# Optimization experiments

Hardware: AMD Instinct MI355X
Metric: run time of the kernel (lower is better)

The kernel has to match this reference:

```python
import jax, jax.numpy as jnp
import numpy as np

N_NODES = 100000
N_EDGES = 1600000
N_PAIRS = 500000
IN_C, HID_C, OUT_C = 128, 128, 128


def setup_inputs() -> dict:
    key = jax.random.key(0)
    ks = jax.random.split(key, 12)
    def lin(k, fan_in, shape):
        b = 1.0 / np.sqrt(fan_in)
        return jax.random.uniform(k, shape, jnp.float32, -b, b)
    return {
        "x": jax.random.normal(ks[0], (N_NODES, IN_C), jnp.float32),
        "edge_index": jax.random.randint(ks[1], (2, N_EDGES), 0, N_NODES),
        "edge_pairs": jax.random.randint(ks[2], (2, N_PAIRS), 0, N_NODES),
        "W1": lin(ks[3], IN_C, (IN_C, HID_C)),
        "b1": jnp.zeros((HID_C,), jnp.float32),
        "W2": lin(ks[4], HID_C, (HID_C, OUT_C)),
        "b2": jnp.zeros((OUT_C,), jnp.float32),
        "Wm1": lin(ks[5], 2 * OUT_C, (2 * OUT_C, HID_C)),
        "bm1": lin(ks[6], 2 * OUT_C, (HID_C,)),
        "Wm2": lin(ks[7], HID_C, (HID_C, 1)),
        "bm2": lin(ks[8], HID_C, (1,)),
    }


def reference(x, edge_index, edge_pairs, W1, b1, W2, b2, Wm1, bm1, Wm2, bm2):
    N = x.shape[0]
    loop = jnp.arange(N, dtype=edge_index.dtype)
    row = jnp.concatenate([edge_index[0], loop])  # source nodes (+self loops)
    col = jnp.concatenate([edge_index[1], loop])  # target nodes (+self loops)
    # symmetric GCN normalization: deg^{-1/2}[row] * deg^{-1/2}[col]
    deg = jax.ops.segment_sum(jnp.ones(col.shape, x.dtype), col, num_segments=N)
    dinv = jnp.where(deg > 0, jax.lax.rsqrt(deg), 0.0)
    norm = dinv[row] * dinv[col]  # [E+N]

    def gcn_conv(h, W, b):
        h = h @ W  # transform first (PyG GCNConv lin has no bias)
        msg = h[row] * norm[:, None]
        return jax.ops.segment_sum(msg, col, num_segments=N) + b

    h = jax.nn.relu(gcn_conv(x, W1, b1))
    h = gcn_conv(h, W2, b2)  # dropout p=0.0 -> identity

    src, dst = edge_pairs[0], edge_pairs[1]
    ef = jnp.concatenate([h[src], h[dst]], axis=-1)  # [P, 2*out]
    out = jax.nn.relu(ef @ Wm1 + bm1) @ Wm2 + bm2
    return out.squeeze(-1)
```

## Files before the change

### kernel.cpp

```cpp
#include <hip/hip_runtime.h>
#include <hip/hip_fp16.h>

#define NCH 128
#define G_NODES 256
#define EPB 4096
#define RCAP 4864
#define MAXNB 512
#define KST 40

typedef __attribute__((ext_vector_type(8))) short short8;
typedef _Float16 half8 __attribute__((ext_vector_type(8)));
typedef __attribute__((ext_vector_type(4))) float floatx4;

static inline size_t align256(size_t x){ return (x + 255) & ~(size_t)255; }

__global__ __launch_bounds__(256) void binA_kernel(
    const int* __restrict__ row, const int* __restrict__ col,
    int* __restrict__ gcur, unsigned* __restrict__ bucketed, int E, int NB,
    const float* __restrict__ W1, const float* __restrict__ W2,
    const float* __restrict__ Wm1, short* __restrict__ planes){
  __shared__ int cnt[MAXNB];
  __shared__ int lbase[MAXNB];
  __shared__ int gbase[MAXNB];
  __shared__ unsigned sorted[EPB];
  __shared__ unsigned short binOf[EPB];
  __shared__ int sh[256];
  __shared__ int carry;
  int t = threadIdx.x;
  int e0 = blockIdx.x * EPB;
  int ecnt = min(EPB, E - e0);
  for (int i = t; i < NB; i += 256) cnt[i] = 0;
  if (t == 0) carry = 0;
  __syncthreads();
  unsigned rec[16]; int bn[16]; int rk[16];
  #pragma unroll
  for (int i = 0; i < 16; i++){
    int e = e0 + i * 256 + t;
    if (e < E){
      int r = row[e], c = col[e];
      bn[i]  = c >> 8;
      rec[i] = (unsigned)r | ((unsigned)(c & 255) << 17);
      rk[i]  = atomicAdd(&cnt[bn[i]], 1);
    } else bn[i] = -1;
  }
  __syncthreads();
  for (int start = 0; start < NB; start += 256){
    int i = start + t;
    int v = (i < NB) ? cnt[i] : 0;
    sh[t] = v; __syncthreads();
    for (int off = 1; off < 256; off <<= 1){
      int val = (t >= off) ? sh[t - off] : 0;
      __syncthreads(); sh[t] += val; __syncthreads();
    }
    if (i < NB) lbase[i] = sh[t] - v + carry;
    __syncthreads();
    if (t == 255) carry += sh[255];
    __syncthreads();
  }
  for (int i = t; i < NB; i += 256){
    int c = cnt[i];
    gbase[i] = (c > 0) ? atomicAdd(&gcur[i], c) : 0;
  }
  __syncthreads();
  #pragma unroll
  for (int i = 0; i < 16; i++){
    if (bn[i] >= 0){
      int pos = lbase[bn[i]] + rk[i];
      sorted[pos] = rec[i];
      binOf[pos]  = (unsigned short)bn[i];
    }
  }
  __syncthreads();
  for (int idx = t; idx < ecnt; idx += 256){
    int b = binOf[idx];
    int gpos = gbase[b] + (idx - lbase[b]);
    if (gpos < RCAP) bucketed[(size_t)b * RCAP + gpos] = sorted[idx];
  }
  {
    int gid = blockIdx.x * 256 + t;
    if (gid < 4 * 16384){
      int mat = gid >> 14;
      int idx = gid & 16383;
      int k = idx >> 7, n = idx & 127;
      const float* src = (mat == 0) ? W1 : (mat == 1) ? W2 : (mat == 2) ? Wm1 : (Wm1 + 16384);
      float x = src[idx];
      short hs, ls;
      if (mat == 0){
        unsigned u = __float_as_uint(x);
        hs = (short)(u >> 16);
        float hf = __uint_as_float(u & 0xFFFF0000u);
        ls = (short)(__float_as_uint(x - hf) >> 16);
      } else {
        __half h = __float2half(x);
        __half l = __float2half(x - __half2float(h));
        hs = __half_as_short(h); ls = __half_as_short(l);
      }
      planes[(size_t)(2 * mat) * 16384 + n * 128 + k]     = hs;
      planes[(size_t)(2 * mat + 1) * 16384 + n * 128 + k] = ls;
    }
  }
}

__global__ __launch_bounds__(512, 4) void fused_gemm_binB(
    const float* __restrict__ X, const short* __restrict__ Whi_,
    const short* __restrict__ Wlo_, __half* __restrict__ O, int nrows, int gemmBlocks,
    const unsigned* __restrict__ bucketed, const int* __restrict__ gcur,
    int* __restrict__ rows_sorted, int* __restrict__ offs,
    int* __restrict__ counts, float* __restrict__ dinv, int N){
  __shared__ __align__(16) char smem[40960];
  int t = threadIdx.x;
  if (blockIdx.x < gemmBlocks){
    short* Xhi = (short*)smem;
    short* Xlo = Xhi + 128 * KST;
    short* Whi = Xlo + 128 * KST;
    short* Wlo = Whi + 128 * KST;
    int w = t >> 6, lane = t & 63;
    int m = lane & 15, q = lane >> 4;
    int row0 = blockIdx.x * 128;
    floatx4 acc[8];
    #pragma unroll
    for (int ct = 0; ct < 8; ct++) acc[ct] = (floatx4)0.f;
    for (int kc = 0; kc < 4; kc++){
      int k0 = kc * 32;
      __syncthreads();
      #pragma unroll
      for (int qq = 0; qq < 2; qq++){
        int f = t + 512 * qq;
        int r = f >> 3, kq = f & 7;
        int gr = row0 + r;
        int grc = (gr < nrows) ? gr : 0;
        float4 v = *(const float4*)(X + (size_t)grc * NCH + k0 + kq * 4);
        short h[4], l[4];
        float vv[4] = {v.x, v.y, v.z, v.w};
        #pragma unroll
        for (int j = 0; j < 4; j++){
          unsigned u = __float_as_uint(vv[j]);
          h[j] = (short)(u >> 16);
          float hf = __uint_as_float(u & 0xFFFF0000u);
          l[j] = (short)(__float_as_uint(vv[j] - hf) >> 16);
        }
        *(uint2*)(Xhi + r * KST + kq * 4) = *(uint2*)h;
        *(uint2*)(Xlo + r * KST + kq * 4) = *(uint2*)l;
      }
      {
        int n = t >> 2, kq = t & 3;
        *(uint4*)(Whi + n * KST + kq * 8) = *(const uint4*)(Whi_ + n * NCH + k0 + kq * 8);
        *(uint4*)(Wlo + n * KST + kq * 8) = *(const uint4*)(Wlo_ + n * NCH + k0 + kq * 8);
      }
      __syncthreads();
      short8 a_hi = *(const short8*)(Xhi + (w * 16 + m) * KST + q * 8);
      short8 a_lo = *(const short8*)(Xlo + (w * 16 + m) * KST + q * 8);
      #pragma unroll
      for (int ct = 0; ct < 8; ct++){
        short8 b_hi = *(const short8*)(Whi + (ct * 16 + m) * KST + q * 8);
        short8 b_lo = *(const short8*)(Wlo + (ct * 16 + m) * KST + q * 8);
        acc[ct] = __builtin_amdgcn_mfma_f32_16x16x32_bf16(a_hi, b_hi, acc[ct], 0, 0, 0);
        acc[ct] = __builtin_amdgcn_mfma_f32_16x16x32_bf16(a_lo, b_hi, acc[ct], 0, 0, 0);
        acc[ct] = __builtin_amdgcn_mfma_f32_16x16x32_bf16(a_hi, b_lo, acc[ct], 0, 0, 0);
      }
    }
    #pragma unroll
    for (int r = 0; r < 4; r++){
      int grow = row0 + w * 16 + q * 4 + r;
      if (grow < nrows){
        #pragma unroll
        for (int ct = 0; ct < 8; ct++)
          O[(size_t)grow * NCH + ct * 16 + m] = __float2half(acc[ct][r]);
      }
    }
  } else {
    int b = blockIdx.x - gemmBlocks;
    unsigned* ledge = (unsigned*)smem;
    int* cnt  = (int*)(smem + RCAP * 4);
    int* cnt2 = cnt + 256;
    int* lex  = cnt2 + 256;
    int* sh   = lex + 256;
    int size = min(gcur[b], RCAP);
    int n0 = b * G_NODES;
    if (t < 256){ cnt[t] = 0; cnt2[t] = 0; }
    __syncthreads();
    for (int i = t; i < size; i += 512){
      unsigned v = bucketed[(size_t)b * RCAP + i];
      ledge[i] = v;
      atomicAdd(&cnt[v >> 17], 1);
    }
    __syncthreads();
    {
      int v = (t < 256) ? cnt[t] : 0;
      if (t < 256) sh[t] = v;
      __syncthreads();
      for (int off = 1; off < 256; off <<= 1){
        int val = (t >= off && t < 256) ? sh[t - off] : 0;
        __syncthreads();
        if (t < 256) sh[t] += val;
        __syncthreads();
      }
      if (t < 256){
        lex[t] = sh[t] - v;
        int n = n0 + t;
        if (n < N){
          counts[n] = v;
          offs[n]   = b * RCAP + sh[t] - v;
          dinv[n]   = rsqrtf((float)v + 1.0f);
        }
      }
    }
    __syncthreads();
    for (int i = t; i < size; i += 512){
      unsigned v = ledge[i];
      int node = v >> 17;
      int pos = lex[node] + atomicAdd(&cnt2[node], 1);
      rows_sorted[(size_t)b * RCAP + pos] = (int)(v & 0x1FFFFu);
    }
  }
}

template<int NCT>
__global__ __launch_bounds__(512, 4) void gemm_f16k(
    const __half* __restrict__ X,
    const short* __restrict__ Whi0, const short* __restrict__ Wlo0,
    const short* __restrict__ Whi1, const short* __restrict__ Wlo1,
    const float* __restrict__ scale, int do_scale,
    __half* __restrict__ O0, __half* __restrict__ O1, int nrows){
  __shared__ short Xs[128 * KST];
  __shared__ short Whs[NCT * 16 * KST];
  __shared__ short Wls[NCT * 16 * KST];
  int t = threadIdx.x;
  int w = t >> 6, lane = t & 63;
  int m = lane & 15, q = lane >> 4;
  int row0 = blockIdx.x * 128;
  floatx4 acc[NCT];
  #pragma unroll
  for (int ct = 0; ct < NCT; ct++) acc[ct] = (floatx4)0.f;

  for (int kc = 0; kc < 4; kc++){
    int k0 = kc * 32;
    __syncthreads();
    {
      int r = t >> 2, kq = t & 3;
      int gr = row0 + r;
      int grc = (gr < nrows) ? gr : 0;
      *(uint4*)(Xs + r * KST + kq * 8) = *(const uint4*)(X + (size_t)grc * NCH + k0 + kq * 8);
    }
    #pragma unroll
    for (int i = t; i < NCT * 16 * 4; i += 512){
      int n = i >> 2, kq = i & 3;
      const short* sh = (n < 128) ? (Whi0 + n * NCH) : (Whi1 + (n - 128) * NCH);
      const short* sl = (n < 128) ? (Wlo0 + n * NCH) : (Wlo1 + (n - 128) * NCH);
      *(uint4*)(Whs + n * KST + kq * 8) = *(const uint4*)(sh + k0 + kq * 8);
      *(uint4*)(Wls + n * KST + kq * 8) = *(const uint4*)(sl + k0 + kq * 8);
    }
    __syncthreads();
    half8 a = *(const half8*)(Xs + (w * 16 + m) * KST + q * 8);
    #pragma unroll
    for (int ct = 0; ct < NCT; ct++){
      half8 bh = *(const half8*)(Whs + (ct * 16 + m) * KST + q * 8);
      half8 bl = *(const half8*)(Wls + (ct * 16 + m) * KST + q * 8);
      acc[ct] = __builtin_amdgcn_mfma_f32_16x16x32_f16(a, bh, acc[ct], 0, 0, 0);
      acc[ct] = __builtin_amdgcn_mfma_f32_16x16x32_f16(a, bl, acc[ct], 0, 0, 0);
    }
  }
  #pragma unroll
  for (int r = 0; r < 4; r++){
    int grow = row0 + w * 16 + q * 4 + r;
    if (grow < nrows){
      float sc = do_scale ? scale[grow] : 1.0f;
      #pragma unroll
      for (int ct = 0; ct < NCT; ct++){
        __half val = __float2half(acc[ct][r] * sc);
        if (ct < 8) O0[(size_t)grow * NCH + ct * 16 + m] = val;
        else        O1[(size_t)grow * NCH + (ct - 8) * 16 + m] = val;
      }
    }
  }
}

__global__ __launch_bounds__(256) void agg_kernel(
    const __half* __restrict__ s, const float* __restrict__ dinv,
    const int* __restrict__ offs, const int* __restrict__ counts,
    const int* __restrict__ rows_sorted, const float* __restrict__ bias,
    __half* __restrict__ outp, int N, int do_relu, int edge_dinv){
  int wave = (int)((blockIdx.x * blockDim.x + threadIdx.x) >> 6);
  int lane = threadIdx.x & 63;
  if (wave >= N) return;
  int c = wave;
  int g = lane >> 4, h = lane & 15;
  float di = dinv[c];
  float wself = edge_dinv ? di : 1.0f;
  float acc[8] = {0.f,0.f,0.f,0.f,0.f,0.f,0.f,0.f};
  if (g == 0){
    uint4 v = *(const uint4*)(s + (size_t)c * NCH + h * 8);
    const __half2* hp = (const __half2*)&v;
    #pragma unroll
    for (int i = 0; i < 4; i++){
      float2 f = __half22float2(hp[i]);
      acc[2*i] = fmaf(wself, f.x, acc[2*i]); acc[2*i+1] = fmaf(wself, f.y, acc[2*i+1]);
    }
  }
  int off = offs[c], cnt = counts[c];
  for (int chunk = 0; chunk < cnt; chunk += 64){
    int nn = min(64, cnt - chunk);
    int myidx = (lane < nn) ? rows_sorted[off + chunk + lane] : 0;
    float mydinv = 1.0f;
    if (edge_dinv && lane < nn) mydinv = dinv[myidx];
    int jmax = (nn + 3) >> 2;
    #pragma unroll 4
    for (int j = 0; j < jmax; j++){
      int e = 4 * j + g;
      int r  = __shfl(myidx, e & 63, 64);
      float dr = edge_dinv ? __shfl(mydinv, e & 63, 64) : 1.0f;
      if (e < nn){
        uint4 v = *(const uint4*)(s + (size_t)r * NCH + h * 8);
        const __half2* hp = (const __half2*)&v;
        #pragma unroll
        for (int i = 0; i < 4; i++){
          float2 f = __half22float2(hp[i]);
          acc[2*i] = fmaf(dr, f.x, acc[2*i]); acc[2*i+1] = fmaf(dr, f.y, acc[2*i+1]);
        }
      }
    }
  }
  #pragma unroll
  for (int i = 0; i < 8; i++){
    acc[i] += __shfl_xor(acc[i], 16, 64);
    acc[i] += __shfl_xor(acc[i], 32, 64);
  }
  if (g == 0){
    float4 b0 = *(const float4*)(bias + h * 8);
    float4 b1 = *(const float4*)(bias + h * 8 + 4);
    float o[8];
    o[0] = di*acc[0]+b0.x; o[1] = di*acc[1]+b0.y; o[2] = di*acc[2]+b0.z; o[3] = di*acc[3]+b0.w;
    o[4] = di*acc[4]+b1.x; o[5] = di*acc[5]+b1.y; o[6] = di*acc[6]+b1.z; o[7] = di*acc[7]+b1.w;
    if (do_relu){
      #pragma unroll
      for (int i = 0; i < 8; i++) o[i] = fmaxf(o[i], 0.f);
    }
    __half2 packed[4];
    #pragma unroll
    for (int i = 0; i < 4; i++) packed[i] = __floats2half2_rn(o[2*i], o[2*i+1]);
    *(uint4*)(outp + (size_t)c * NCH + h * 8) = *(uint4*)packed;
  }
}

__global__ __launch_bounds__(256) void pair_kernel(
    const __half* __restrict__ A, const __half* __restrict__ B,
    const int* __restrict__ src, const int* __restrict__ dst,
    const float* __restrict__ bm1, const float* __restrict__ Wm2,
    const float* __restrict__ bm2, float* __restrict__ outp, int P){
  int gwave = (int)((blockIdx.x * blockDim.x + threadIdx.x) >> 6);
  int lane  = threadIdx.x & 63;
  int nw    = (int)((gridDim.x * blockDim.x) >> 6);
  int g = lane >> 4, h = lane & 15;
  float bb[8], ww[8];
  {
    float4 t0 = *(const float4*)(bm1 + h * 8);
    float4 t1 = *(const float4*)(bm1 + h * 8 + 4);
    bb[0]=t0.x; bb[1]=t0.y; bb[2]=t0.z; bb[3]=t0.w;
    bb[4]=t1.x; bb[5]=t1.y; bb[6]=t1.z; bb[7]=t1.w;
    float4 w0 = *(const float4*)(Wm2 + h * 8);
    float4 w1 = *(const float4*)(Wm2 + h * 8 + 4);
    ww[0]=w0.x; ww[1]=w0.y; ww[2]=w0.z; ww[3]=w0.w;
    ww[4]=w1.x; ww[5]=w1.y; ww[6]=w1.z; ww[7]=w1.w;
  }
  float bsc = bm2[0];
  const __half* basep = (g & 1) ? B : A;
  const int* idxp = (g & 1) ? dst : src;
  for (int p0 = gwave * 4; p0 < P; p0 += nw * 4){
    int piA = p0 + (g >> 1);
    int piB = p0 + 2 + (g >> 1);
    int piAX = (piA < P) ? piA : P - 1;
    int piBX = (piB < P) ? piB : P - 1;
    int nodeA = idxp[piAX];
    int nodeB = idxp[piBX];
    uint4 vA = *(const uint4*)(basep + (size_t)nodeA * NCH + h * 8);
    uint4 vB = *(const uint4*)(basep + (size_t)nodeB * NCH + h * 8);
    const __half2* hpA = (const __half2*)&vA;
    const __half2* hpB = (const __half2*)&vB;
    float fA[8], fB[8];
    #pragma unroll
    for (int i = 0; i < 4; i++){
      float2 ta = __half22float2(hpA[i]);
      float2 tb = __half22float2(hpB[i]);
      fA[2*i] = ta.x; fA[2*i+1] = ta.y;
      fB[2*i] = tb.x; fB[2*i+1] = tb.y;
    }
    float pA = 0.f, pB = 0.f;
    #pragma unroll
    for (int i = 0; i < 8; i++){
      float oA = __shfl_xor(fA[i], 16, 64);
      float oB = __shfl_xor(fB[i], 16, 64);
      float zA = fmaxf(fA[i] + oA + bb[i], 0.f);
      float zB = fmaxf(fB[i] + oB + bb[i], 0.f);
      pA += zA * ww[i];
      pB += zB * ww[i];
    }
    #pragma unroll
    for (int d = 1; d <= 8; d <<= 1){
      pA += __shfl_xor(pA, d, 64);
      pB += __shfl_xor(pB, d, 64);
    }
    if ((lane & 31) == 0){
      if (piA < P) outp[piA] = pA + bsc;
      if (piB < P) outp[piB] = pB + bsc;
    }
  }
}


extern "C" void kernel_launch(void* const* d_in, const int* in_sizes, int n_in,
                              void* d_out, int out_size, void* d_ws, size_t ws_size,
                              hipStream_t stream){
  const float* x   = (const float*)d_in[0];
  const int*   ei  = (const int*)  d_in[1];
  const int*   ep  = (const int*)  d_in[2];
  const float* W1  = (const float*)d_in[3];
  const float* b1  = (const float*)d_in[4];
  const float* W2  = (const float*)d_in[5];
  const float* b2  = (const float*)d_in[6];
  const float* Wm1 = (const float*)d_in[7];
  const float* bm1 = (const float*)d_in[8];
  const float* Wm2 = (const float*)d_in[9];
  const float* bm2 = (const float*)d_in[10];
  float* outp = (float*)d_out;

  const int N = in_sizes[0] / NCH;
  const int E = in_sizes[1] / 2;
  const int P = in_sizes[2] / 2;
  const int NB = (N + G_NODES - 1) / G_NODES;

  char* base = (char*)d_ws;
  size_t off = 0;
  int*      counts      = (int*)     (base + off); off = align256(off + (size_t)N * 4);
  int*      offs        = (int*)     (base + off); off = align256(off + (size_t)N * 4);
  float*    dinv        = (float*)   (base + off); off = align256(off + (size_t)N * 4);
  int*      gcur        = (int*)     (base + off); off = align256(off + (size_t)NB * 4);
  unsigned* bucketed    = (unsigned*)(base + off); off = align256(off + (size_t)NB * RCAP * 4);
  int*      rows_sorted = (int*)     (base + off); off = align256(off + (size_t)NB * RCAP * 4);
  short*    planes      = (short*)   (base + off); off = align256(off + (size_t)8 * 16384 * 2);
  __half*   s1buf       = (__half*)  (base + off); off = align256(off + (size_t)N * NCH * 2);
  __half*   h1buf       = (__half*)  (base + off); off = align256(off + (size_t)N * NCH * 2);
  __half*   s2buf       = (__half*)  (base + off); off = align256(off + (size_t)N * NCH * 2);
  __half*   sA          = (__half*)  (base + off); off = align256(off + (size_t)N * NCH * 2);
  __half*   sB          = (__half*)  (base + off); off = align256(off + (size_t)N * NCH * 2);
  (void)ws_size; (void)n_in; (void)out_size;

  short* W1hi = planes + 0 * 16384;
  short* W1lo = planes + 1 * 16384;
  short* W2hi = planes + 2 * 16384;
  short* W2lo = planes + 3 * 16384;
  short* Wahi = planes + 4 * 16384;
  short* Walo = planes + 5 * 16384;
  short* Wbhi = planes + 6 * 16384;
  short* Wblo = planes + 7 * 16384;

  const int* row = ei;
  const int* col = ei + E;
  const int* psrc = ep;
  const int* pdst = ep + P;

  int gemm_grid = (N + 127) / 128;
  int agg_grid  = (N + 3) / 4;

  hipMemsetAsync(gcur, 0, (size_t)NB * 4, stream);
  binA_kernel<<<(E + EPB - 1) / EPB, 256, 0, stream>>>(row, col, gcur, bucketed, E, NB,
                                                       W1, W2, Wm1, planes);
  fused_gemm_binB<<<gemm_grid + NB, 512, 0, stream>>>(
      x, W1hi, W1lo, s1buf, N, gemm_grid,
      bucketed, gcur, rows_sorted, offs, counts, dinv, N);
  agg_kernel<<<agg_grid, 256, 0, stream>>>(s1buf, dinv, offs, counts, rows_sorted, b1, h1buf, N, 1, 1);
  gemm_f16k<8><<<gemm_grid, 512, 0, stream>>>(h1buf, W2hi, W2lo, W2hi, W2lo, dinv, 1, s2buf, s2buf, N);
  agg_kernel<<<agg_grid, 256, 0, stream>>>(s2buf, dinv, offs, counts, rows_sorted, b2, h1buf, N, 0, 0);
  gemm_f16k<16><<<gemm_grid, 512, 0, stream>>>(h1buf, Wahi, Walo, Wbhi, Wblo, dinv, 0, sA, sB, N);
  pair_kernel<<<8192, 256, 0, stream>>>(sA, sB, psrc, pdst, bm1, Wm2, bm2, outp, P);
}
```

Baseline: 383.7 us.

## Store GCN features in 16-channel slices and aggregate per slice

Intermediate GCN feature buffers move from row-major [N][128] to a sliced [8][N][16] layout, written by the first-layer and second-layer GEMMs and read by the GEMM that follows each aggregation. A new templated aggregation kernel gives each node four threads within one 16-channel slice, with blockIdx selecting the slice, and loops serially over the node's neighbours. Edge indices, offsets and counts use nontemporal loads, and outputs use nontemporal stores. The aim is a smaller gather working set per slice and better cache locality, at the cost of reading the edge list eight times and using narrower 8-byte gathers.

```diff
diff --git a/kernel.cpp b/kernel.cpp
--- a/kernel.cpp
+++ b/kernel.cpp
@@ -7,6 +7,7 @@
 #define RCAP 4864
 #define MAXNB 512
 #define KST 40
+#define NSLICE 8
 
 typedef __attribute__((ext_vector_type(8))) short short8;
 typedef _Float16 half8 __attribute__((ext_vector_type(8)));
@@ -165,7 +166,7 @@
       if (grow < nrows){
         #pragma unroll
         for (int ct = 0; ct < 8; ct++)
-          O[(size_t)grow * NCH + ct * 16 + m] = __float2half(acc[ct][r]);
+          O[((size_t)ct * nrows + grow) * 16 + m] = __float2half(acc[ct][r]);
       }
     }
   } else {
@@ -240,7 +241,9 @@
       int r = t >> 2, kq = t & 3;
       int gr = row0 + r;
       int grc = (gr < nrows) ? gr : 0;
-      *(uint4*)(Xs + r * KST + kq * 8) = *(const uint4*)(X + (size_t)grc * NCH + k0 + kq * 8);
+      int k = k0 + kq * 8;
+      *(uint4*)(Xs + r * KST + kq * 8) =
+        *(const uint4*)(X + ((size_t)(k >> 4) * nrows + grc) * 16 + (k & 15));
     }
     #pragma unroll
     for (int i = t; i < NCT * 16 * 4; i += 512){
@@ -268,77 +271,73 @@
       #pragma unroll
       for (int ct = 0; ct < NCT; ct++){
         __half val = __float2half(acc[ct][r] * sc);
-        if (ct < 8) O0[(size_t)grow * NCH + ct * 16 + m] = val;
-        else        O1[(size_t)grow * NCH + (ct - 8) * 16 + m] = val;
-      }
-    }
-  }
-}
-
-__global__ __launch_bounds__(256) void agg_kernel(
+        if (NCT == 8){
+          O0[((size_t)ct * nrows + grow) * 16 + m] = val;
+        } else {
+          if (ct < 8) O0[(size_t)grow * NCH + ct * 16 + m] = val;
+          else        O1[(size_t)grow * NCH + (ct - 8) * 16 + m] = val;
+        }
+      }
+    }
+  }
+}
+
+template<int EDGE_DINV>
+__global__ __launch_bounds__(256) void agg_slice_kernel(
     const __half* __restrict__ s, const float* __restrict__ dinv,
     const int* __restrict__ offs, const int* __restrict__ counts,
     const int* __restrict__ rows_sorted, const float* __restrict__ bias,
-    __half* __restrict__ outp, int N, int do_relu, int edge_dinv){
-  int wave = (int)((blockIdx.x * blockDim.x + threadIdx.x) >> 6);
-  int lane = threadIdx.x & 63;
-  if (wave >= N) return;
-  int c = wave;
-  int g = lane >> 4, h = lane & 15;
-  float di = dinv[c];
-  float wself = edge_dinv ? di : 1.0f;
-  float acc[8] = {0.f,0.f,0.f,0.f,0.f,0.f,0.f,0.f};
-  if (g == 0){
-    uint4 v = *(const uint4*)(s + (size_t)c * NCH + h * 8);
-    const __half2* hp = (const __half2*)&v;
-    #pragma unroll
-    for (int i = 0; i < 4; i++){
-      float2 f = __half22float2(hp[i]);
-      acc[2*i] = fmaf(wself, f.x, acc[2*i]); acc[2*i+1] = fmaf(wself, f.y, acc[2*i+1]);
-    }
-  }
-  int off = offs[c], cnt = counts[c];
-  for (int chunk = 0; chunk < cnt; chunk += 64){
-    int nn = min(64, cnt - chunk);
-    int myidx = (lane < nn) ? rows_sorted[off + chunk + lane] : 0;
-    float mydinv = 1.0f;
-    if (edge_dinv && lane < nn) mydinv = dinv[myidx];
-    int jmax = (nn + 3) >> 2;
-    #pragma unroll 4
-    for (int j = 0; j < jmax; j++){
-      int e = 4 * j + g;
-      int r  = __shfl(myidx, e & 63, 64);
-      float dr = edge_dinv ? __shfl(mydinv, e & 63, 64) : 1.0f;
-      if (e < nn){
-        uint4 v = *(const uint4*)(s + (size_t)r * NCH + h * 8);
+    __half* __restrict__ outp, int N, int do_relu, int ngroups){
+  const int slice = blockIdx.x & 7;
+  const int t = threadIdx.x;
+  const int grp = t >> 2;
+  const int j = t & 3;
+  const __half* sbase = s + (size_t)slice * N * 16;
+  __half* obase = outp + (size_t)slice * N * 16;
+  const float4 bv = *(const float4*)(bias + slice * 16 + j * 4);
+  const int gstep = gridDim.x >> 3;
+  for (int g = blockIdx.x >> 3; g < ngroups; g += gstep){
+    int c = g * 64 + grp;
+    if (c < N){
+      float di = dinv[c];
+      float wself = EDGE_DINV ? di : 1.0f;
+      int off = __builtin_nontemporal_load(offs + c);
+      int cnt = __builtin_nontemporal_load(counts + c);
+      float a0, a1, a2, a3;
+      {
+        uint2 v = *(const uint2*)(sbase + (size_t)c * 16 + j * 4);
         const __half2* hp = (const __half2*)&v;
-        #pragma unroll
-        for (int i = 0; i < 4; i++){
-          float2 f = __half22float2(hp[i]);
-          acc[2*i] = fmaf(dr, f.x, acc[2*i]); acc[2*i+1] = fmaf(dr, f.y, acc[2*i+1]);
-        }
-      }
-    }
-  }
-  #pragma unroll
-  for (int i = 0; i < 8; i++){
-    acc[i] += __shfl_xor(acc[i], 16, 64);
-    acc[i] += __shfl_xor(acc[i], 32, 64);
-  }
-  if (g == 0){
-    float4 b0 = *(const float4*)(bias + h * 8);
-    float4 b1 = *(const float4*)(bias + h * 8 + 4);
-    float o[8];
-    o[0] = di*acc[0]+b0.x; o[1] = di*acc[1]+b0.y; o[2] = di*acc[2]+b0.z; o[3] = di*acc[3]+b0.w;
-    o[4] = di*acc[4]+b1.x; o[5] = di*acc[5]+b1.y; o[6] = di*acc[6]+b1.z; o[7] = di*acc[7]+b1.w;
-    if (do_relu){
-      #pragma unroll
-      for (int i = 0; i < 8; i++) o[i] = fmaxf(o[i], 0.f);
-    }
-    __half2 packed[4];
-    #pragma unroll
-    for (int i = 0; i < 4; i++) packed[i] = __floats2half2_rn(o[2*i], o[2*i+1]);
-    *(uint4*)(outp + (size_t)c * NCH + h * 8) = *(uint4*)packed;
+        float2 f0 = __half22float2(hp[0]);
+        float2 f1 = __half22float2(hp[1]);
+        a0 = wself * f0.x; a1 = wself * f0.y;
+        a2 = wself * f1.x; a3 = wself * f1.y;
+      }
+      const int* rp = rows_sorted + off;
+      #pragma unroll 4
+      for (int e = 0; e < cnt; e++){
+        int r = __builtin_nontemporal_load(rp + e);
+        float dr = EDGE_DINV ? dinv[r] : 1.0f;
+        uint2 v = *(const uint2*)(sbase + (size_t)r * 16 + j * 4);
+        const __half2* hp = (const __half2*)&v;
+        float2 f0 = __half22float2(hp[0]);
+        float2 f1 = __half22float2(hp[1]);
+        a0 = fmaf(dr, f0.x, a0); a1 = fmaf(dr, f0.y, a1);
+        a2 = fmaf(dr, f1.x, a2); a3 = fmaf(dr, f1.y, a3);
+      }
+      float o0 = di * a0 + bv.x, o1 = di * a1 + bv.y;
+      float o2 = di * a2 + bv.z, o3 = di * a3 + bv.w;
+      if (do_relu){
+        o0 = fmaxf(o0, 0.f); o1 = fmaxf(o1, 0.f);
+        o2 = fmaxf(o2, 0.f); o3 = fmaxf(o3, 0.f);
+      }
+      __half2 p0 = __floats2half2_rn(o0, o1);
+      __half2 p1 = __floats2half2_rn(o2, o3);
+      unsigned long long pk =
+        (unsigned long long)*(unsigned*)&p0 |
+        ((unsigned long long)*(unsigned*)&p1 << 32);
+      __builtin_nontemporal_store(pk,
+        (unsigned long long*)(obase + (size_t)c * 16 + j * 4));
+    }
   }
 }
 
@@ -459,7 +458,7 @@
   const int* pdst = ep + P;
 
   int gemm_grid = (N + 127) / 128;
-  int agg_grid  = (N + 3) / 4;
+  int ngroups   = (N + 63) / 64;
 
   hipMemsetAsync(gcur, 0, (size_t)NB * 4, stream);
   binA_kernel<<<(E + EPB - 1) / EPB, 256, 0, stream>>>(row, col, gcur, bucketed, E, NB,
@@ -467,9 +466,11 @@
   fused_gemm_binB<<<gemm_grid + NB, 512, 0, stream>>>(
       x, W1hi, W1lo, s1buf, N, gemm_grid,
       bucketed, gcur, rows_sorted, offs, counts, dinv, N);
-  agg_kernel<<<agg_grid, 256, 0, stream>>>(s1buf, dinv, offs, counts, rows_sorted, b1, h1buf, N, 1, 1);
+  agg_slice_kernel<1><<<2048, 256, 0, stream>>>(s1buf, dinv, offs, counts, rows_sorted,
+                                                b1, h1buf, N, 1, ngroups);
   gemm_f16k<8><<<gemm_grid, 512, 0, stream>>>(h1buf, W2hi, W2lo, W2hi, W2lo, dinv, 1, s2buf, s2buf, N);
-  agg_kernel<<<agg_grid, 256, 0, stream>>>(s2buf, dinv, offs, counts, rows_sorted, b2, h1buf, N, 0, 0);
+  agg_slice_kernel<0><<<2048, 256, 0, stream>>>(s2buf, dinv, offs, counts, rows_sorted,
+                                                b2, h1buf, N, 0, ngroups);
   gemm_f16k<16><<<gemm_grid, 512, 0, stream>>>(h1buf, Wahi, Walo, Wbhi, Wblo, dinv, 0, sA, sB, N);
   pair_kernel<<<8192, 256, 0, stream>>>(sA, sB, psrc, pdst, bm1, Wm2, bm2, outp, P);
 }
```

Result: slower. 599.7 us (+56.3%).
